# Kernel tuning notes

Hardware: AMD Instinct MI355X
Metric: run time of the kernel (lower is better)

Reference implementation:

```python
import jax, jax.numpy as jnp
import numpy as np

NUM_PTS = 8   # num_points_per_face
K = 5         # self.k


def _sq_dist(x, y):
    # squared euclidean distance matrix (Nx, Ny); matches torch.cdist**2 / sum((a-b)**2)
    x2 = jnp.sum(x * x, axis=1)[:, None]
    y2 = jnp.sum(y * y, axis=1)[None, :]
    d = x2 + y2 - 2.0 * (x @ y.T)
    return jnp.maximum(d, 0.0)


def setup_inputs() -> dict:
    key = jax.random.key(0)
    k1, k2, k3, k4, k5, k6, k7 = jax.random.split(key, 7)
    V, Fs, Ft = 2048, 4096, 4096
    return {
        "source_vertices": jax.random.normal(k1, (1, V, 3), dtype=jnp.float32),
        "source_faces": jax.random.randint(k2, (Fs, 3), 0, V),
        "target_vertices": jax.random.normal(k3, (1, V, 3), dtype=jnp.float32),
        "target_faces": jax.random.randint(k4, (3, Ft), 0, V),
        "face_probs": jax.random.uniform(k5, (Fs,), dtype=jnp.float32),
        "r1u": jax.random.uniform(k6, (Fs, NUM_PTS), dtype=jnp.float32),
        "r2u": jax.random.uniform(k7, (Fs, NUM_PTS), dtype=jnp.float32),
    }


def reference(source_vertices, source_faces, target_vertices, target_faces, face_probs, r1u, r2u):
    sv = source_vertices[0]                 # (V, 3)
    tv = target_vertices[0]                 # (V, 3)
    tf = target_faces.T                     # (Ft, 3)
    Fs = source_faces.shape[0]

    src_bc = sv[source_faces].mean(axis=1)  # (Fs, 3) source barycenters
    tgt_bc = tv[tf].mean(axis=1)            # (Ft, 3) target barycenters

    # ---- forward loss: prob-weighted min squared distance to target barycenters
    d_fwd = _sq_dist(src_bc, tgt_bc)        # (Fs, Ft)
    forward_loss = jnp.sum(face_probs * jnp.min(d_fwd, axis=1))

    # ---- sample points from triangles via barycentric coords
    r1 = jnp.sqrt(r1u)
    w1 = 1.0 - r1
    w2 = r1 * (1.0 - r2u)
    w3 = r1 * r2u
    v1 = sv[source_faces[:, 0]]             # (Fs, 3)
    v2 = sv[source_faces[:, 1]]
    v3 = sv[source_faces[:, 2]]
    pts = (w1[..., None] * v1[:, None] + w2[..., None] * v2[:, None]
           + w3[..., None] * v3[:, None]).reshape(-1, 3)   # (P, 3), P = Fs*NUM_PTS
    pt_faces = jnp.repeat(jnp.arange(Fs), NUM_PTS)          # (P,)
    pt_probs = face_probs[pt_faces]                         # (P,)

    # ---- reverse loss, batched over all P points
    d_src = _sq_dist(pts, src_bc)                           # (P, Fs)
    neg_d, idx = jax.lax.top_k(-d_src, K + 1)               # K+1 smallest distances
    tri_dists = -neg_d                                      # (P, K+1)
    mask = idx != pt_faces[:, None]                         # exclude own face
    has_self = jnp.any(~mask, axis=1)
    excl_pos = jnp.where(has_self, jnp.argmin(mask, axis=1), K + 1)  # (P,)
    t = jnp.arange(K)
    sel = t[None, :] + (t[None, :] >= excl_pos[:, None]).astype(jnp.int32)  # (P, K)
    valid_dists = jnp.take_along_axis(tri_dists, sel, axis=1)   # (P, K)
    valid_idx = jnp.take_along_axis(idx, sel, axis=1)           # (P, K)
    valid_probs = face_probs[valid_idx]                         # (P, K)

    min_tgt = jnp.min(_sq_dist(pts, tgt_bc), axis=1)            # (P,)

    reverse_loss = jnp.sum(pt_probs * min_tgt
                           + (1.0 - pt_probs) * jnp.mean(valid_probs * valid_dists, axis=1))
    return forward_loss + reverse_loss
```

## Files before the change

### kernel.cpp

```cpp
#include <hip/hip_runtime.h>
#include <math.h>

#define FS 4096
#define FT 4096
#define TS 512
#define NPH 4
#define NPT 32768
#define BIGF 3.0e38f
#define KEYINF 0xFFFFFFFFu

typedef float v2f __attribute__((ext_vector_type(2)));

__device__ __forceinline__ unsigned umin32(unsigned a, unsigned b) { return a < b ? a : b; }
__device__ __forceinline__ unsigned umax32(unsigned a, unsigned b) { return a < b ? b : a; }

__device__ __forceinline__ unsigned med3u(unsigned a, unsigned b, unsigned c) {
    unsigned d;
    asm("v_med3_u32 %0, %1, %2, %3" : "=v"(d) : "v"(a), "v"(b), "v"(c));
    return d;
}

__device__ __forceinline__ unsigned and_or(unsigned a, unsigned m, unsigned o) {
    unsigned d;
    asm("v_and_or_b32 %0, %1, %2, %3" : "=v"(d) : "v"(a), "v"(m), "v"(o));
    return d;
}

__device__ __forceinline__ v2f pk_add(v2f a, v2f b) {
    v2f d;
    asm("v_pk_add_f32 %0, %1, %2" : "=v"(d) : "v"(a), "v"(b));
    return d;
}
__device__ __forceinline__ v2f pk_fma(v2f a, v2f b, v2f c) {
    v2f d;
    asm("v_pk_fma_f32 %0, %1, %2, %3" : "=v"(d) : "v"(a), "v"(b), "v"(c));
    return d;
}
__device__ __forceinline__ void pk_fma_acc(v2f& d, v2f a, v2f b) {
    asm("v_pk_fma_f32 %0, %1, %2, %0" : "+v"(d) : "v"(a), "v"(b));
}

__device__ __forceinline__ void gl_lds16(const float4* g, float4* l) {
    __builtin_amdgcn_global_load_lds(
        (__attribute__((address_space(1))) void*)(g),
        (__attribute__((address_space(3))) void*)(l), 16, 0, 0);
}

__device__ __forceinline__ float block_reduce_sum(float v) {
    __shared__ float s[8];
    for (int o = 32; o > 0; o >>= 1) v += __shfl_down(v, o, 64);
    int lane = threadIdx.x & 63, wid = threadIdx.x >> 6;
    if (lane == 0) s[wid] = v;
    __syncthreads();
    int nw = blockDim.x >> 6;
    v = (threadIdx.x < (unsigned)nw) ? s[threadIdx.x] : 0.f;
    if (wid == 0)
        for (int o = 4; o > 0; o >>= 1) v += __shfl_down(v, o, 64);
    return v;
}

#define CE(x, y) { unsigned _n = umin32(x, y); y = umax32(x, y); x = _n; }

__device__ __forceinline__ void merge32(unsigned s[6]) {
    #pragma unroll
    for (int m = 1; m <= 16; m <<= 1) {
        unsigned b0 = __shfl_xor(s[0], m, 64), b1 = __shfl_xor(s[1], m, 64);
        unsigned b2 = __shfl_xor(s[2], m, 64), b3 = __shfl_xor(s[3], m, 64);
        unsigned b4 = __shfl_xor(s[4], m, 64), b5 = __shfl_xor(s[5], m, 64);
        unsigned l0 = s[0], l1 = s[1];
        unsigned l2 = umin32(s[2], b5), l3 = umin32(s[3], b4);
        unsigned l4 = umin32(s[4], b3), l5 = umin32(s[5], b2);
        unsigned l6 = b1, l7 = b0;
        CE(l0, l4) CE(l1, l5) CE(l2, l6) CE(l3, l7)
        CE(l0, l2) CE(l1, l3) CE(l4, l6) CE(l5, l7)
        CE(l0, l1) CE(l2, l3) CE(l4, l5) CE(l6, l7)
        s[0] = l0; s[1] = l1; s[2] = l2; s[3] = l3; s[4] = l4; s[5] = l5;
    }
}

__global__ __launch_bounds__(64) void k_prep(
        const float* __restrict__ sv, const int* __restrict__ sf,
        const float* __restrict__ tv, const int* __restrict__ tf,
        float4* __restrict__ sbc2, float4* __restrict__ tbc2,
        float4* __restrict__ sbcr, float* __restrict__ out) {
    int i = blockIdx.x * 64 + threadIdx.x;
    if (i == 0) out[0] = 0.f;
    if (i >= FS) return;
    const float third = 1.f / 3.f;
    int a = sf[3*i], b = sf[3*i+1], c = sf[3*i+2];
    float x = (sv[3*a  ] + sv[3*b  ] + sv[3*c  ]) * third;
    float y = (sv[3*a+1] + sv[3*b+1] + sv[3*c+1]) * third;
    float z = (sv[3*a+2] + sv[3*b+2] + sv[3*c+2]) * third;
    float n2 = x*x + y*y + z*z;
    sbcr[i] = make_float4(x, y, z, n2);
    int ta = tf[i], tb = tf[FT + i], tc = tf[2*FT + i];
    float tx = (tv[3*ta  ] + tv[3*tb  ] + tv[3*tc  ]) * third;
    float ty = (tv[3*ta+1] + tv[3*tb+1] + tv[3*tc+1]) * third;
    float tz = (tv[3*ta+2] + tv[3*tb+2] + tv[3*tc+2]) * third;
    float tn2 = tx*tx + ty*ty + tz*tz;

    int tt = i >> 10, cc = i & 1023;
    int g = cc >> 6, half = (cc >> 5) & 1, pp = cc & 31;
    int lo4 = tt*1024 + g*32 + pp, hi4 = lo4 + 512;
    float* S = (float*)sbc2;
    S[4*lo4 + half]     = -2.f*x;  S[4*lo4 + 2 + half] = -2.f*y;
    S[4*hi4 + half]     = -2.f*z;  S[4*hi4 + 2 + half] = n2;
    float* T = (float*)tbc2;
    T[4*lo4 + half]     = -2.f*tx; T[4*lo4 + 2 + half] = -2.f*ty;
    T[4*hi4 + half]     = -2.f*tz; T[4*hi4 + 2 + half] = tn2;
}

__global__ __launch_bounds__(256) void k_main(
        const float* __restrict__ sv, const int* __restrict__ sf,
        const float* __restrict__ r1u, const float* __restrict__ r2u,
        const float4* __restrict__ sbc2, const float4* __restrict__ tbc2,
        unsigned* __restrict__ rvk, float* __restrict__ rvm,
        float* __restrict__ pp2v, float* __restrict__ fwdv) {
    __shared__ float4 tileS[TS];
    __shared__ float4 tileT[TS];
    int tid  = threadIdx.x;
    int seg  = tid & 31;
    int slot = tid >> 5;

    if (blockIdx.x < 2048) {
        int half = blockIdx.x & 1;
        int pg   = blockIdx.x >> 1;
        int pt0  = pg * 32 + slot * 4;
        int face = pt0 >> 3;

        int a = sf[3*face], b = sf[3*face+1], c = sf[3*face+2];
        float ax = sv[3*a], ay = sv[3*a+1], az = sv[3*a+2];
        float bx = sv[3*b], by = sv[3*b+1], bz = sv[3*b+2];
        float cx = sv[3*c], cy = sv[3*c+1], cz = sv[3*c+2];
        float4 r14 = ((const float4*)r1u)[pt0 >> 2];
        float4 r24 = ((const float4*)r2u)[pt0 >> 2];
        v2f pxb[4], pyb[4], pzb[4], p2b[4];
        {
            float r1a[4] = {r14.x, r14.y, r14.z, r14.w};
            float r2a[4] = {r24.x, r24.y, r24.z, r24.w};
            #pragma unroll
            for (int i = 0; i < 4; ++i) {
                float r1 = sqrtf(r1a[i]);
                float w1 = 1.f - r1, w2 = r1 * (1.f - r2a[i]), w3 = r1 * r2a[i];
                float px = w1*ax + w2*bx + w3*cx;
                float py = w1*ay + w2*by + w3*cy;
                float pz = w1*az + w2*bz + w3*cz;
                float p2 = px*px + py*py + pz*pz;
                pxb[i] = (v2f){px, px}; pyb[i] = (v2f){py, py};
                pzb[i] = (v2f){pz, pz}; p2b[i] = (v2f){p2, p2};
            }
        }

        unsigned s0[4], s1[4], s2[4];
        #pragma unroll
        for (int i = 0; i < 4; ++i) { s0[i]=KEYINF; s1[i]=KEYINF; s2[i]=KEYINF; }
        v2f vm2[4];
        #pragma unroll
        for (int i = 0; i < 4; ++i) vm2[i] = (v2f){BIGF, BIGF};

        unsigned kMask = 0xFFFFF000u;

        for (int p = 0; p < NPH; ++p) {
            int pp  = half * NPH + p;
            int loB = ((pp >> 1) << 10) + ((pp & 1) << 8);
            __syncthreads();
            gl_lds16(&sbc2[loB + tid],       &tileS[tid]);
            gl_lds16(&sbc2[loB + 512 + tid], &tileS[256 + tid]);
            gl_lds16(&tbc2[loB + tid],       &tileT[tid]);
            gl_lds16(&tbc2[loB + 512 + tid], &tileT[256 + tid]);
            __syncthreads();
            unsigned jja = (unsigned)(pp * TS + seg);
            #pragma unroll 4
            for (int g = 0; g < 8; ++g) {
                float4 lo = tileS[(g << 5) + seg];
                float4 hi = tileS[256 + (g << 5) + seg];
                v2f cx2 = {lo.x, lo.y}, cy2 = {lo.z, lo.w};
                v2f cz2 = {hi.x, hi.y}, cw2 = {hi.z, hi.w};
                #pragma unroll
                for (int i = 0; i < 4; ++i) {
                    v2f d2 = pk_add(cw2, p2b[i]);
                    pk_fma_acc(d2, pzb[i], cz2);
                    pk_fma_acc(d2, pyb[i], cy2);
                    pk_fma_acc(d2, pxb[i], cx2);
                    unsigned ka = and_or(__float_as_uint(d2.x), kMask, jja);
                    unsigned kb = and_or(__float_as_uint(d2.y), kMask, jja + 32u);
                    unsigned n0 = umin32(s0[i], ka);
                    unsigned n1 = med3u(s0[i], s1[i], ka);
                    unsigned n2 = med3u(s1[i], s2[i], ka);
                    s0[i]=n0; s1[i]=n1; s2[i]=n2;
                    n0 = umin32(s0[i], kb);
                    n1 = med3u(s0[i], s1[i], kb);
                    n2 = med3u(s1[i], s2[i], kb);
                    s0[i]=n0; s1[i]=n1; s2[i]=n2;
                }
                jja += 64;
            }
            #pragma unroll 4
            for (int g = 0; g < 8; ++g) {
                float4 lo = tileT[(g << 5) + seg];
                float4 hi = tileT[256 + (g << 5) + seg];
                v2f cx2 = {lo.x, lo.y}, cy2 = {lo.z, lo.w};
                v2f cz2 = {hi.x, hi.y}, cw2 = {hi.z, hi.w};
                #pragma unroll
                for (int i = 0; i < 4; ++i) {
                    v2f t = pk_fma(pzb[i], cz2, cw2);
                    pk_fma_acc(t, pyb[i], cy2);
                    pk_fma_acc(t, pxb[i], cx2);
                    vm2[i].x = fminf(vm2[i].x, t.x);
                    vm2[i].y = fminf(vm2[i].y, t.y);
                }
            }
        }

        float vm[4];
        #pragma unroll
        for (int i = 0; i < 4; ++i) {
            float v = fminf(vm2[i].x, vm2[i].y);
            v = fminf(v, __shfl_xor(v, 1, 64));
            v = fminf(v, __shfl_xor(v, 2, 64));
            v = fminf(v, __shfl_xor(v, 4, 64));
            v = fminf(v, __shfl_xor(v, 8, 64));
            v = fminf(v, __shfl_xor(v, 16, 64));
            vm[i] = v;
        }

        #pragma unroll
        for (int i = 0; i < 4; ++i) {
            unsigned srt[6] = {s0[i], s1[i], s2[i], KEYINF, KEYINF, KEYINF};
            merge32(srt);
            if (seg == 0) {
                int pt = pt0 + i;
                unsigned* kb = rvk + half * 6 * NPT + pt;
                kb[0]       = srt[0];  kb[NPT]   = srt[1];
                kb[2*NPT]   = srt[2];  kb[3*NPT] = srt[3];
                kb[4*NPT]   = srt[4];  kb[5*NPT] = srt[5];
                rvm[half * NPT + pt] = vm[i];
                if (half == 0) pp2v[pt] = p2b[i].x;
            }
        }
    } else {
        int idx  = blockIdx.x - 2048;
        int half = idx & 1;
        int fg   = idx >> 1;
        int f0   = fg * 32 + slot * 4;
        const float4* sbcr = tbc2 + FS;
        float4 q0, q1, q2, q3;
        {
            #pragma unroll
            for (int i = 0; i < 4; ++i) {
                int f = f0 + i;
                int tt = f >> 10, cc = f & 1023;
                int g = cc >> 6, hh = (cc >> 5) & 1, ppn = cc & 31;
                int lo4 = tt*1024 + g*32 + ppn, hi4 = lo4 + 512;
                const float* S = (const float*)sbc2;
                float x = -0.5f * S[4*lo4 + hh];
                float y = -0.5f * S[4*lo4 + 2 + hh];
                float z = -0.5f * S[4*hi4 + hh];
                float w =         S[4*hi4 + 2 + hh];
                float4 q = make_float4(x, y, z, w);
                if (i == 0) q0 = q; else if (i == 1) q1 = q;
                else if (i == 2) q2 = q; else q3 = q;
            }
        }
        float qw[4] = {q0.w, q1.w, q2.w, q3.w};
        v2f qxb[4] = {{q0.x,q0.x},{q1.x,q1.x},{q2.x,q2.x},{q3.x,q3.x}};
        v2f qyb[4] = {{q0.y,q0.y},{q1.y,q1.y},{q2.y,q2.y},{q3.y,q3.y}};
        v2f qzb[4] = {{q0.z,q0.z},{q1.z,q1.z},{q2.z,q2.z},{q3.z,q3.z}};
        v2f vf2[4];
        #pragma unroll
        for (int i = 0; i < 4; ++i) vf2[i] = (v2f){BIGF, BIGF};

        for (int p = 0; p < NPH; ++p) {
            int pp  = half * NPH + p;
            int loB = ((pp >> 1) << 10) + ((pp & 1) << 8);
            __syncthreads();
            gl_lds16(&tbc2[loB + tid],       &tileT[tid]);
            gl_lds16(&tbc2[loB + 512 + tid], &tileT[256 + tid]);
            __syncthreads();
            #pragma unroll 4
            for (int g = 0; g < 8; ++g) {
                float4 lo = tileT[(g << 5) + seg];
                float4 hi = tileT[256 + (g << 5) + seg];
                v2f cx2 = {lo.x, lo.y}, cy2 = {lo.z, lo.w};
                v2f cz2 = {hi.x, hi.y}, cw2 = {hi.z, hi.w};
                #pragma unroll
                for (int i = 0; i < 4; ++i) {
                    v2f t = pk_fma(qzb[i], cz2, cw2);
                    pk_fma_acc(t, qyb[i], cy2);
                    pk_fma_acc(t, qxb[i], cx2);
                    vf2[i].x = fminf(vf2[i].x, t.x);
                    vf2[i].y = fminf(vf2[i].y, t.y);
                }
            }
        }
        #pragma unroll
        for (int i = 0; i < 4; ++i) {
            float v = fminf(vf2[i].x, vf2[i].y);
            v = fminf(v, __shfl_xor(v, 1, 64));
            v = fminf(v, __shfl_xor(v, 2, 64));
            v = fminf(v, __shfl_xor(v, 4, 64));
            v = fminf(v, __shfl_xor(v, 8, 64));
            v = fminf(v, __shfl_xor(v, 16, 64));
            if (seg == 0) fwdv[half * FS + f0 + i] = v;
        }
    }
}

__global__ __launch_bounds__(256) void k_merge(
        const float* __restrict__ fp, const float4* __restrict__ sbcr,
        const unsigned* __restrict__ rvk, const float* __restrict__ rvm,
        const float* __restrict__ pp2v, const float* __restrict__ fwdv,
        float* __restrict__ out) {
    int tid = threadIdx.x;
    float contrib = 0.f;
    if (blockIdx.x < 128) {
        int pt = blockIdx.x * 256 + tid;
        int face = pt >> 3;
        unsigned a0 = rvk[pt],         a1 = rvk[NPT + pt];
        unsigned a2 = rvk[2*NPT + pt], a3 = rvk[3*NPT + pt];
        unsigned a4 = rvk[4*NPT + pt], a5 = rvk[5*NPT + pt];
        unsigned b0 = rvk[6*NPT + pt], b1 = rvk[7*NPT + pt];
        unsigned b2 = rvk[8*NPT + pt], b3 = rvk[9*NPT + pt];
        unsigned b4 = rvk[10*NPT + pt], b5 = rvk[11*NPT + pt];
        a0 = umin32(a0, b5); a1 = umin32(a1, b4); a2 = umin32(a2, b3);
        a3 = umin32(a3, b2); a4 = umin32(a4, b1); a5 = umin32(a5, b0);
        float vm = fminf(rvm[pt], rvm[NPT + pt]);
        float p2 = pp2v[pt];
        float pf = fp[face];
        unsigned mx = umax32(umax32(umax32(a0, a1), umax32(a2, a3)),
                             umax32(a4, a5));
        float ss = 0.f; unsigned ex = mx;
        {
            int q; float d;
            q = a0 & 0xFFF; d = __uint_as_float(a0 & 0xFFFFF000u);
            ss += fp[q] * d; if (q == face) ex = a0;
            q = a1 & 0xFFF; d = __uint_as_float(a1 & 0xFFFFF000u);
            ss += fp[q] * d; if (q == face) ex = a1;
            q = a2 & 0xFFF; d = __uint_as_float(a2 & 0xFFFFF000u);
            ss += fp[q] * d; if (q == face) ex = a2;
            q = a3 & 0xFFF; d = __uint_as_float(a3 & 0xFFFFF000u);
            ss += fp[q] * d; if (q == face) ex = a3;
            q = a4 & 0xFFF; d = __uint_as_float(a4 & 0xFFFFF000u);
            ss += fp[q] * d; if (q == face) ex = a4;
            q = a5 & 0xFFF; d = __uint_as_float(a5 & 0xFFFFF000u);
            ss += fp[q] * d; if (q == face) ex = a5;
        }
        ss -= fp[ex & 0xFFF] * __uint_as_float(ex & 0xFFFFF000u);
        float mtd = fmaxf(vm + p2, 0.f);
        contrib = pf * mtd + (1.f - pf) * (ss * 0.2f);
    } else {
        int f = (blockIdx.x - 128) * 256 + tid;
        float vf = fminf(fwdv[f], fwdv[FS + f]);
        float qw = ((const float*)sbcr)[4*f + 3];
        contrib = fp[f] * fmaxf(vf + qw, 0.f);
    }
    float tot = block_reduce_sum(contrib);
    if (tid == 0) atomicAdd(out, tot);
}

extern "C" void kernel_launch(void* const* d_in, const int* in_sizes, int n_in,
                              void* d_out, int out_size, void* d_ws, size_t ws_size,
                              hipStream_t stream) {
    const float* sv  = (const float*)d_in[0];
    const int*   sf  = (const int*)  d_in[1];
    const float* tv  = (const float*)d_in[2];
    const int*   tf  = (const int*)  d_in[3];
    const float* fp  = (const float*)d_in[4];
    const float* r1u = (const float*)d_in[5];
    const float* r2u = (const float*)d_in[6];
    float* out = (float*)d_out;

    char* ws = (char*)d_ws;
    float4*   sbc2 = (float4*)(ws);
    float4*   tbc2 = (float4*)(ws + 65536);
    float4*   sbcr = (float4*)(ws + 131072);
    unsigned* rvk  = (unsigned*)(ws + 196608);
    float*    rvm  = (float*)(ws + 196608 + 1572864);
    float*    pp2v = (float*)(ws + 2031616);
    float*    fwdv = (float*)(ws + 2162688);

    k_prep <<<64,   64,  0, stream>>>(sv, sf, tv, tf, sbc2, tbc2, sbcr, out);
    k_main <<<2304, 256, 0, stream>>>(sv, sf, r1u, r2u, sbc2, tbc2,
                                      rvk, rvm, pp2v, fwdv);
    k_merge<<<144,  256, 0, stream>>>(fp, sbcr, rvk, rvm, pp2v, fwdv, out);
}
```

Baseline: 116.7 us.

## Split reverse-pass candidates four ways with eight points per thread

```diff
diff --git a/kernel.cpp b/kernel.cpp
--- a/kernel.cpp
+++ b/kernel.cpp
@@ -4,7 +4,6 @@
 #define FS 4096
 #define FT 4096
 #define TS 512
-#define NPH 4
 #define NPT 32768
 #define BIGF 3.0e38f
 #define KEYINF 0xFFFFFFFFu
@@ -123,23 +122,27 @@
     int slot = tid >> 5;
 
     if (blockIdx.x < 2048) {
-        int half = blockIdx.x & 1;
-        int pg   = blockIdx.x >> 1;
-        int pt0  = pg * 32 + slot * 4;
+        int q    = blockIdx.x & 3;
+        int pg   = blockIdx.x >> 2;
+        int pt0  = pg * 64 + slot * 8;
         int face = pt0 >> 3;
 
         int a = sf[3*face], b = sf[3*face+1], c = sf[3*face+2];
         float ax = sv[3*a], ay = sv[3*a+1], az = sv[3*a+2];
         float bx = sv[3*b], by = sv[3*b+1], bz = sv[3*b+2];
         float cx = sv[3*c], cy = sv[3*c+1], cz = sv[3*c+2];
-        float4 r14 = ((const float4*)r1u)[pt0 >> 2];
-        float4 r24 = ((const float4*)r2u)[pt0 >> 2];
-        v2f pxb[4], pyb[4], pzb[4], p2b[4];
+        float4 r14a = ((const float4*)r1u)[pt0 >> 2];
+        float4 r14b = ((const float4*)r1u)[(pt0 >> 2) + 1];
+        float4 r24a = ((const float4*)r2u)[pt0 >> 2];
+        float4 r24b = ((const float4*)r2u)[(pt0 >> 2) + 1];
+        v2f pxb[8], pyb[8], pzb[8], p2b[8];
         {
-            float r1a[4] = {r14.x, r14.y, r14.z, r14.w};
-            float r2a[4] = {r24.x, r24.y, r24.z, r24.w};
+            float r1a[8] = {r14a.x, r14a.y, r14a.z, r14a.w,
+                            r14b.x, r14b.y, r14b.z, r14b.w};
+            float r2a[8] = {r24a.x, r24a.y, r24a.z, r24a.w,
+                            r24b.x, r24b.y, r24b.z, r24b.w};
             #pragma unroll
-            for (int i = 0; i < 4; ++i) {
+            for (int i = 0; i < 8; ++i) {
                 float r1 = sqrtf(r1a[i]);
                 float w1 = 1.f - r1, w2 = r1 * (1.f - r2a[i]), w3 = r1 * r2a[i];
                 float px = w1*ax + w2*bx + w3*cx;
@@ -151,33 +154,33 @@
             }
         }
 
-        unsigned s0[4], s1[4], s2[4];
-        #pragma unroll
-        for (int i = 0; i < 4; ++i) { s0[i]=KEYINF; s1[i]=KEYINF; s2[i]=KEYINF; }
-        v2f vm2[4];
-        #pragma unroll
-        for (int i = 0; i < 4; ++i) vm2[i] = (v2f){BIGF, BIGF};
+        unsigned s0[8], s1[8], s2[8];
+        #pragma unroll
+        for (int i = 0; i < 8; ++i) { s0[i]=KEYINF; s1[i]=KEYINF; s2[i]=KEYINF; }
+        v2f vm2[8];
+        #pragma unroll
+        for (int i = 0; i < 8; ++i) vm2[i] = (v2f){BIGF, BIGF};
 
         unsigned kMask = 0xFFFFF000u;
 
-        for (int p = 0; p < NPH; ++p) {
-            int pp  = half * NPH + p;
-            int loB = ((pp >> 1) << 10) + ((pp & 1) << 8);
+        for (int p = 0; p < 2; ++p) {
+            int gp  = q * 2 + p;
+            int loB = ((gp >> 1) << 10) + ((gp & 1) << 8);
             __syncthreads();
             gl_lds16(&sbc2[loB + tid],       &tileS[tid]);
             gl_lds16(&sbc2[loB + 512 + tid], &tileS[256 + tid]);
             gl_lds16(&tbc2[loB + tid],       &tileT[tid]);
             gl_lds16(&tbc2[loB + 512 + tid], &tileT[256 + tid]);
             __syncthreads();
-            unsigned jja = (unsigned)(pp * TS + seg);
-            #pragma unroll 4
+            unsigned jja = (unsigned)(gp * TS + seg);
+            #pragma unroll 2
             for (int g = 0; g < 8; ++g) {
                 float4 lo = tileS[(g << 5) + seg];
                 float4 hi = tileS[256 + (g << 5) + seg];
                 v2f cx2 = {lo.x, lo.y}, cy2 = {lo.z, lo.w};
                 v2f cz2 = {hi.x, hi.y}, cw2 = {hi.z, hi.w};
                 #pragma unroll
-                for (int i = 0; i < 4; ++i) {
+                for (int i = 0; i < 8; ++i) {
                     v2f d2 = pk_add(cw2, p2b[i]);
                     pk_fma_acc(d2, pzb[i], cz2);
                     pk_fma_acc(d2, pyb[i], cy2);
@@ -195,14 +198,14 @@
                 }
                 jja += 64;
             }
-            #pragma unroll 4
+            #pragma unroll 2
             for (int g = 0; g < 8; ++g) {
                 float4 lo = tileT[(g << 5) + seg];
                 float4 hi = tileT[256 + (g << 5) + seg];
                 v2f cx2 = {lo.x, lo.y}, cy2 = {lo.z, lo.w};
                 v2f cz2 = {hi.x, hi.y}, cw2 = {hi.z, hi.w};
                 #pragma unroll
-                for (int i = 0; i < 4; ++i) {
+                for (int i = 0; i < 8; ++i) {
                     v2f t = pk_fma(pzb[i], cz2, cw2);
                     pk_fma_acc(t, pyb[i], cy2);
                     pk_fma_acc(t, pxb[i], cx2);
@@ -212,9 +215,9 @@
             }
         }
 
-        float vm[4];
-        #pragma unroll
-        for (int i = 0; i < 4; ++i) {
+        float vm[8];
+        #pragma unroll
+        for (int i = 0; i < 8; ++i) {
             float v = fminf(vm2[i].x, vm2[i].y);
             v = fminf(v, __shfl_xor(v, 1, 64));
             v = fminf(v, __shfl_xor(v, 2, 64));
@@ -225,17 +228,17 @@
         }
 
         #pragma unroll
-        for (int i = 0; i < 4; ++i) {
+        for (int i = 0; i < 8; ++i) {
             unsigned srt[6] = {s0[i], s1[i], s2[i], KEYINF, KEYINF, KEYINF};
             merge32(srt);
             if (seg == 0) {
                 int pt = pt0 + i;
-                unsigned* kb = rvk + half * 6 * NPT + pt;
-                kb[0]       = srt[0];  kb[NPT]   = srt[1];
-                kb[2*NPT]   = srt[2];  kb[3*NPT] = srt[3];
-                kb[4*NPT]   = srt[4];  kb[5*NPT] = srt[5];
-                rvm[half * NPT + pt] = vm[i];
-                if (half == 0) pp2v[pt] = p2b[i].x;
+                unsigned* kb = rvk + q * 6 * NPT + pt;
+                kb[0]     = srt[0];  kb[NPT]   = srt[1];
+                kb[2*NPT] = srt[2];  kb[3*NPT] = srt[3];
+                kb[4*NPT] = srt[4];  kb[5*NPT] = srt[5];
+                rvm[q * NPT + pt] = vm[i];
+                if (q == 0) pp2v[pt] = p2b[i].x;
             }
         }
     } else {
@@ -243,7 +246,6 @@
         int half = idx & 1;
         int fg   = idx >> 1;
         int f0   = fg * 32 + slot * 4;
-        const float4* sbcr = tbc2 + FS;
         float4 q0, q1, q2, q3;
         {
             #pragma unroll
@@ -257,12 +259,11 @@
                 float y = -0.5f * S[4*lo4 + 2 + hh];
                 float z = -0.5f * S[4*hi4 + hh];
                 float w =         S[4*hi4 + 2 + hh];
-                float4 q = make_float4(x, y, z, w);
-                if (i == 0) q0 = q; else if (i == 1) q1 = q;
-                else if (i == 2) q2 = q; else q3 = q;
-            }
-        }
-        float qw[4] = {q0.w, q1.w, q2.w, q3.w};
+                float4 qq = make_float4(x, y, z, w);
+                if (i == 0) q0 = qq; else if (i == 1) q1 = qq;
+                else if (i == 2) q2 = qq; else q3 = qq;
+            }
+        }
         v2f qxb[4] = {{q0.x,q0.x},{q1.x,q1.x},{q2.x,q2.x},{q3.x,q3.x}};
         v2f qyb[4] = {{q0.y,q0.y},{q1.y,q1.y},{q2.y,q2.y},{q3.y,q3.y}};
         v2f qzb[4] = {{q0.z,q0.z},{q1.z,q1.z},{q2.z,q2.z},{q3.z,q3.z}};
@@ -270,9 +271,9 @@
         #pragma unroll
         for (int i = 0; i < 4; ++i) vf2[i] = (v2f){BIGF, BIGF};
 
-        for (int p = 0; p < NPH; ++p) {
-            int pp  = half * NPH + p;
-            int loB = ((pp >> 1) << 10) + ((pp & 1) << 8);
+        for (int p = 0; p < 4; ++p) {
+            int gp  = half * 4 + p;
+            int loB = ((gp >> 1) << 10) + ((gp & 1) << 8);
             __syncthreads();
             gl_lds16(&tbc2[loB + tid],       &tileT[tid]);
             gl_lds16(&tbc2[loB + 512 + tid], &tileT[256 + tid]);
@@ -316,34 +317,44 @@
     if (blockIdx.x < 128) {
         int pt = blockIdx.x * 256 + tid;
         int face = pt >> 3;
-        unsigned a0 = rvk[pt],         a1 = rvk[NPT + pt];
-        unsigned a2 = rvk[2*NPT + pt], a3 = rvk[3*NPT + pt];
-        unsigned a4 = rvk[4*NPT + pt], a5 = rvk[5*NPT + pt];
-        unsigned b0 = rvk[6*NPT + pt], b1 = rvk[7*NPT + pt];
-        unsigned b2 = rvk[8*NPT + pt], b3 = rvk[9*NPT + pt];
-        unsigned b4 = rvk[10*NPT + pt], b5 = rvk[11*NPT + pt];
-        a0 = umin32(a0, b5); a1 = umin32(a1, b4); a2 = umin32(a2, b3);
-        a3 = umin32(a3, b2); a4 = umin32(a4, b1); a5 = umin32(a5, b0);
-        float vm = fminf(rvm[pt], rvm[NPT + pt]);
+        const unsigned* K = rvk + pt;
+        unsigned a0 = K[0],     a1 = K[NPT],   a2 = K[2*NPT];
+        unsigned a3 = K[3*NPT], a4 = K[4*NPT], a5 = K[5*NPT];
+        #pragma unroll
+        for (int q = 1; q < 4; ++q) {
+            const unsigned* Kq = K + q * 6 * NPT;
+            #pragma unroll
+            for (int j = 0; j < 6; ++j) {
+                unsigned k = Kq[j * NPT];
+                unsigned n0 = umin32(a0, k);
+                unsigned n1 = med3u(a0, a1, k);
+                unsigned n2 = med3u(a1, a2, k);
+                unsigned n3 = med3u(a2, a3, k);
+                unsigned n4 = med3u(a3, a4, k);
+                unsigned n5 = med3u(a4, a5, k);
+                a0=n0; a1=n1; a2=n2; a3=n3; a4=n4; a5=n5;
+            }
+        }
+        float vm = fminf(fminf(rvm[pt],         rvm[NPT + pt]),
+                         fminf(rvm[2*NPT + pt], rvm[3*NPT + pt]));
         float p2 = pp2v[pt];
         float pf = fp[face];
-        unsigned mx = umax32(umax32(umax32(a0, a1), umax32(a2, a3)),
-                             umax32(a4, a5));
-        float ss = 0.f; unsigned ex = mx;
+        unsigned ex = a5;
+        float ss = 0.f;
         {
-            int q; float d;
-            q = a0 & 0xFFF; d = __uint_as_float(a0 & 0xFFFFF000u);
-            ss += fp[q] * d; if (q == face) ex = a0;
-            q = a1 & 0xFFF; d = __uint_as_float(a1 & 0xFFFFF000u);
-            ss += fp[q] * d; if (q == face) ex = a1;
-            q = a2 & 0xFFF; d = __uint_as_float(a2 & 0xFFFFF000u);
-            ss += fp[q] * d; if (q == face) ex = a2;
-            q = a3 & 0xFFF; d = __uint_as_float(a3 & 0xFFFFF000u);
-            ss += fp[q] * d; if (q == face) ex = a3;
-            q = a4 & 0xFFF; d = __uint_as_float(a4 & 0xFFFFF000u);
-            ss += fp[q] * d; if (q == face) ex = a4;
-            q = a5 & 0xFFF; d = __uint_as_float(a5 & 0xFFFFF000u);
-            ss += fp[q] * d; if (q == face) ex = a5;
+            int qi; float d;
+            qi = a0 & 0xFFF; d = __uint_as_float(a0 & 0xFFFFF000u);
+            ss += fp[qi] * d; if (qi == face) ex = a0;
+            qi = a1 & 0xFFF; d = __uint_as_float(a1 & 0xFFFFF000u);
+            ss += fp[qi] * d; if (qi == face) ex = a1;
+            qi = a2 & 0xFFF; d = __uint_as_float(a2 & 0xFFFFF000u);
+            ss += fp[qi] * d; if (qi == face) ex = a2;
+            qi = a3 & 0xFFF; d = __uint_as_float(a3 & 0xFFFFF000u);
+            ss += fp[qi] * d; if (qi == face) ex = a3;
+            qi = a4 & 0xFFF; d = __uint_as_float(a4 & 0xFFFFF000u);
+            ss += fp[qi] * d; if (qi == face) ex = a4;
+            qi = a5 & 0xFFF; d = __uint_as_float(a5 & 0xFFFFF000u);
+            ss += fp[qi] * d; if (qi == face) ex = a5;
         }
         ss -= fp[ex & 0xFFF] * __uint_as_float(ex & 0xFFFFF000u);
         float mtd = fmaxf(vm + p2, 0.f);
@@ -375,9 +386,9 @@
     float4*   tbc2 = (float4*)(ws + 65536);
     float4*   sbcr = (float4*)(ws + 131072);
     unsigned* rvk  = (unsigned*)(ws + 196608);
-    float*    rvm  = (float*)(ws + 196608 + 1572864);
-    float*    pp2v = (float*)(ws + 2031616);
-    float*    fwdv = (float*)(ws + 2162688);
+    float*    rvm  = (float*)(ws + 3342336);
+    float*    pp2v = (float*)(ws + 3866624);
+    float*    fwdv = (float*)(ws + 3997696);
 
     k_prep <<<64,   64,  0, stream>>>(sv, sf, tv, tf, sbc2, tbc2, sbcr, out);
     k_main <<<2304, 256, 0, stream>>>(sv, sf, r1u, r2u, sbc2, tbc2,
```

Measured after the change: 126.5 us. +8.4%, slower.
